# Kernel optimization log

Measured on AMD Instinct MI355X. Metric: run time of the kernel, lower is better.

Reference implementation:

```python
import jax, jax.numpy as jnp
import numpy as np

D_MODEL, D_STATE, DT_RANK = 768, 16, 48
D_INNER = 2 * D_MODEL
B, L = 2, 1024


def ste_clamp(x, lo, hi):
    return x + jax.lax.stop_gradient(jnp.clip(x, lo, hi) - x)


def bitlinear(x, w):
    """BitNet-b1.58-style BitLinear: ternary weights (absmean scale) +
    int8 absmax activation quantization, both with straight-through estimators."""
    eps = 1e-6
    sw = jnp.mean(jnp.abs(w)) + eps
    wn = w / sw
    wq = wn + jax.lax.stop_gradient(jnp.round(jnp.clip(wn, -1.0, 1.0)) - wn)
    sx = 127.0 / (jnp.max(jnp.abs(x), axis=-1, keepdims=True) + eps)
    xn = x * sx
    xq = xn + jax.lax.stop_gradient(jnp.round(jnp.clip(xn, -128.0, 127.0)) - xn)
    return (xq @ wq.T) * (sw / sx)


def bitshift_norm(x, gamma):
    # RMS norm where 1/rms is snapped to a power of two (bit-shift)
    xc = x - jnp.mean(x, axis=-1, keepdims=True)
    var = jnp.mean(xc * xc, axis=-1, keepdims=True)
    rms = jnp.sqrt(var + 1e-6)
    k = jnp.clip(jnp.round(jnp.log2(rms)), 0.0, None)
    inv_rms = 2.0 ** (-k)
    return xc * inv_rms * gamma


def depthwise_conv1d(x, w, b):
    # x: [B, L, C]; w: [C, 1, 4]; b: [C] -> [B, L+3, C] (padding=3 both sides, kernel 4)
    y = jax.lax.conv_general_dilated(
        x.transpose(0, 2, 1), w, window_strides=(1,), padding=[(3, 3)],
        feature_group_count=x.shape[-1], dimension_numbers=("NCH", "OIH", "NCH"))
    return (y + b[None, :, None]).transpose(0, 2, 1)


def dyadic_scan(u, decay):
    # h_t = decay_t * h_{t-1} + u_t along axis=1, vectorized via associative scan
    def combine(c1, c2):
        a1, b1 = c1
        a2, b2 = c2
        return a1 * a2, b1 * a2 + b2
    _, h = jax.lax.associative_scan(combine, (decay, u), axis=1)
    return h


def setup_inputs() -> dict:
    key = jax.random.key(0)
    ks = jax.random.split(key, 8)
    return {
        "hidden_states": jax.random.normal(ks[0], (B, L, D_MODEL), jnp.float32),
        "gamma": jnp.ones((D_MODEL,), jnp.float32),
        "in_proj_w": 0.02 * jax.random.normal(ks[1], (2 * D_INNER, D_MODEL), jnp.float32),
        "conv_w": 0.1 * jax.random.normal(ks[2], (D_INNER, 1, 4), jnp.float32),
        "conv_b": 0.01 * jax.random.normal(ks[3], (D_INNER,), jnp.float32),
        "x_proj_w": 0.02 * jax.random.normal(ks[4], (DT_RANK + 2 * D_STATE, D_INNER), jnp.float32),
        "dt_proj_w": 0.02 * jax.random.normal(ks[5], (D_INNER, DT_RANK), jnp.float32),
        "out_proj_w": 0.02 * jax.random.normal(ks[6], (D_MODEL, D_INNER), jnp.float32),
        "base_decay_nums": jnp.full((D_INNER, D_STATE), 28000.0, jnp.float32),
        "res_gate": jnp.full((1,), 0.01, jnp.float32),
        "decay_shifts": jnp.full((D_INNER, D_STATE), 15.0, jnp.float32),
    }


def reference(hidden_states, gamma, in_proj_w, conv_w, conv_b, x_proj_w,
              dt_proj_w, out_proj_w, base_decay_nums, res_gate, decay_shifts):
    residual = hidden_states
    hs = hidden_states - jnp.mean(hidden_states, axis=-1, keepdims=True)  # module-level centering
    hs = bitshift_norm(hs, gamma)

    xz = bitlinear(hs, in_proj_w)
    x, z = jnp.split(xz, 2, axis=-1)                      # each [B, L, D_INNER]
    x = depthwise_conv1d(x, conv_w, conv_b)[:, :L]
    x = jnp.clip(x, -50.0, 50.0)
    x = 0.5 * (x + jnp.sqrt(x * x + 4.0))                 # smooth softplus-like

    proj = bitlinear(x, x_proj_w)
    dt, B_ssm, C_ssm = jnp.split(proj, [DT_RANK, DT_RANK + D_STATE], axis=-1)
    decay_mod = bitlinear(dt, dt_proj_w)                  # [B, L, D_INNER]

    decay_nums = ste_clamp(base_decay_nums[None, None] + decay_mod[..., None], 0.0, 32000.0)
    dt_val = ste_clamp(0.5 * (decay_mod + jnp.sqrt(decay_mod * decay_mod + 4.0)) * 0.01, 0.0, 0.1)

    u = (x * dt_val)[..., None] * B_ssm[:, :, None, :]    # [B, L, D_INNER, N]
    Bs, Ls, Din, N = u.shape
    u_flat = jnp.clip(u.reshape(Bs, Ls, Din * N), -100.0, 100.0)
    dn_flat = decay_nums.reshape(Bs, Ls, Din * N)
    decay = dn_flat * (2.0 ** (-decay_shifts.reshape(-1)))  # [B, L, Din*N]

    h_flat = jnp.clip(dyadic_scan(u_flat, decay), -1000.0, 1000.0)
    h = h_flat.reshape(Bs, Ls, Din, N)

    y = jnp.einsum("bldn,bln->bld", h, C_ssm)
    y = y * (0.5 * (z / jnp.sqrt(z * z + 1.0) + 1.0))     # smooth sigmoid gate
    out = bitlinear(y, out_proj_w)
    return residual + out * res_gate
```

## Files before the change

kernel.cpp:

```cpp
#include <hip/hip_runtime.h>
#include <hip/hip_bf16.h>
#include <math.h>

#define D_MODEL 768
#define D_STATE 16
#define DT_RANK 48
#define D_INNER 1536
#define XZ_DIM  3072
#define PROJ_DIM 80
#define Bb 2
#define Ll 1024
#define ROWS (Bb*Ll)

#define OFF_PART   0u
#define OFF_SW     256u
#define OFF_WQIN   512u
#define OFF_WQXPT  (OFF_WQIN  + 2359296u)
#define OFF_WQDT   (OFF_WQXPT + 122880u)
#define OFF_WQOUT  (OFF_WQDT  + 73728u)
#define OFF_XQ1    (OFF_WQOUT + 1179648u)
#define OFF_S1     (OFF_XQ1   + 1572864u)
#define OFF_XZ     (OFF_S1    + 2048u)
#define OFF_XS     (OFF_XZ    + 6291456u)
#define OFF_YG     (OFF_XS    + 3145728u)
#define OFF_S2     (OFF_YG    + 3145728u)
#define OFF_PROJ   (OFF_S2    + 2048u)
#define OFF_XQ3    (OFF_PROJ  + 163840u)
#define OFF_S3     (OFF_XQ3   + 98304u)
#define OFF_DMX    (OFF_S3    + 2048u)
#define OFF_XQ4    (OFF_DMX   + 6291456u)
#define OFF_S4     (OFF_XQ4   + 3145728u)

typedef short sh8 __attribute__((ext_vector_type(8)));
typedef float f32x4 __attribute__((ext_vector_type(4)));

#define N_IN_W  (XZ_DIM * D_MODEL)
#define N_XP_W  (PROJ_DIM * D_INNER)
#define N_DT_P  (D_INNER * 64)
#define N_OUT_W (D_MODEL * D_INNER)

__device__ __forceinline__ float blk_sum(float v, float* sm) {
    int tid = threadIdx.x;
    #pragma unroll
    for (int off = 32; off; off >>= 1) v += __shfl_down(v, off);
    __syncthreads();
    if ((tid & 63) == 0) sm[tid >> 6] = v;
    __syncthreads();
    return (sm[0] + sm[1]) + (sm[2] + sm[3]);
}
__device__ __forceinline__ float blk_max(float v, float* sm) {
    int tid = threadIdx.x;
    #pragma unroll
    for (int off = 32; off; off >>= 1) v = fmaxf(v, __shfl_down(v, off));
    __syncthreads();
    if ((tid & 63) == 0) sm[tid >> 6] = v;
    __syncthreads();
    return fmaxf(fmaxf(sm[0], sm[1]), fmaxf(sm[2], sm[3]));
}
__device__ __forceinline__ float clampf(float v, float lo, float hi) {
    return fminf(fmaxf(v, lo), hi);
}
__device__ __forceinline__ void gload_lds16(const __hip_bfloat16* g, __hip_bfloat16* l) {
    __builtin_amdgcn_global_load_lds(
        (const __attribute__((address_space(1))) void*)g,
        (__attribute__((address_space(3))) void*)l, 16, 0, 0);
}
__device__ __forceinline__ float red16_dpp(float v) {
    int t;
    t = __builtin_amdgcn_update_dpp(0, __float_as_int(v), 0xB1,  0xF, 0xF, true);
    v += __int_as_float(t);
    t = __builtin_amdgcn_update_dpp(0, __float_as_int(v), 0x4E,  0xF, 0xF, true);
    v += __int_as_float(t);
    t = __builtin_amdgcn_update_dpp(0, __float_as_int(v), 0x124, 0xF, 0xF, true);
    v += __int_as_float(t);
    t = __builtin_amdgcn_update_dpp(0, __float_as_int(v), 0x128, 0xF, 0xF, true);
    v += __int_as_float(t);
    return v;
}

__global__ __launch_bounds__(256) void absmean_all(
    const float* __restrict__ w0, const float* __restrict__ w1,
    const float* __restrict__ w2, const float* __restrict__ w3,
    float* __restrict__ part) {
    __shared__ float sm[4];
    int bid = blockIdx.x;
    const float* w; int n, sub, nb;
    if (bid < 512)      { w = w0; n = N_IN_W;           sub = bid;       nb = 512; }
    else if (bid < 576) { w = w1; n = N_XP_W;           sub = bid - 512; nb = 64;  }
    else if (bid < 640) { w = w2; n = D_INNER*DT_RANK;  sub = bid - 576; nb = 64;  }
    else                { w = w3; n = N_OUT_W;          sub = bid - 640; nb = 384; }
    float sum = 0.f;
    for (int i = sub * 256 + threadIdx.x; i < n; i += nb * 256)
        sum += fabsf(w[i]);
    sum = blk_sum(sum, sm);
    if (threadIdx.x == 0) part[bid] = sum;
}

__global__ __launch_bounds__(256) void absmean_final4(
    const float* __restrict__ part, float* __restrict__ sw) {
    __shared__ float sm[4];
    int tid = threadIdx.x;
    const int cnt[4] = {512, 64, 64, 384};
    const int off[4] = {0, 512, 576, 640};
    const int ns[4]  = {N_IN_W, N_XP_W, D_INNER*DT_RANK, N_OUT_W};
    #pragma unroll
    for (int m = 0; m < 4; ++m) {
        float v = 0.f;
        for (int i = tid; i < cnt[m]; i += 256) v += part[off[m] + i];
        v = blk_sum(v, sm);
        if (tid == 0) sw[m] = v / (float)ns[m] + 1e-6f;
    }
}

__global__ void quant_all(const float* __restrict__ w_in, const float* __restrict__ w_xp,
                          const float* __restrict__ w_dt, const float* __restrict__ w_out,
                          const float* __restrict__ sw,
                          __hip_bfloat16* __restrict__ wqin, float* __restrict__ wqxpT,
                          __hip_bfloat16* __restrict__ wqdt, __hip_bfloat16* __restrict__ wqout) {
    int idx = blockIdx.x * 256 + threadIdx.x;
    if (idx < N_IN_W) {
        float v = rintf(clampf(w_in[idx] / sw[0], -1.f, 1.f));
        wqin[idx] = __float2bfloat16(v);
    } else if (idx < N_IN_W + N_XP_W) {
        int i = idx - N_IN_W;
        int j = i / D_INNER, k = i % D_INNER;
        wqxpT[k * PROJ_DIM + j] = rintf(clampf(w_xp[i] / sw[1], -1.f, 1.f));
    } else if (idx < N_IN_W + N_XP_W + N_DT_P) {
        int i = idx - N_IN_W - N_XP_W;
        int r = i >> 6, c = i & 63;
        float v = (c < DT_RANK) ? rintf(clampf(w_dt[r * DT_RANK + c] / sw[2], -1.f, 1.f)) : 0.f;
        wqdt[i] = __float2bfloat16(v);
    } else if (idx < N_IN_W + N_XP_W + N_DT_P + N_OUT_W) {
        int i = idx - N_IN_W - N_XP_W - N_DT_P;
        float v = rintf(clampf(w_out[i] / sw[3], -1.f, 1.f));
        wqout[i] = __float2bfloat16(v);
    }
}

__global__ __launch_bounds__(256) void norm_quant(
    const float* __restrict__ x, const float* __restrict__ gamma,
    const float* __restrict__ swp, __hip_bfloat16* __restrict__ xq, float* __restrict__ s1) {
    int row = blockIdx.x, tid = threadIdx.x;
    const float* xr = x + (size_t)row * D_MODEL;
    __shared__ float sm[4];
    float v0 = xr[tid], v1 = xr[tid + 256], v2 = xr[tid + 512];
    float m1 = blk_sum(v0 + v1 + v2, sm) * (1.f / D_MODEL);
    v0 -= m1; v1 -= m1; v2 -= m1;
    float m2 = blk_sum(v0 + v1 + v2, sm) * (1.f / D_MODEL);
    v0 -= m2; v1 -= m2; v2 -= m2;
    float var = blk_sum(v0 * v0 + v1 * v1 + v2 * v2, sm) * (1.f / D_MODEL);
    float rms = sqrtf(var + 1e-6f);
    float k = fmaxf(rintf(log2f(rms)), 0.f);
    float inv = exp2f(-k);
    float g0 = gamma[tid], g1 = gamma[tid + 256], g2 = gamma[tid + 512];
    float h0 = v0 * inv * g0, h1 = v1 * inv * g1, h2 = v2 * inv * g2;
    float mx = blk_max(fmaxf(fabsf(h0), fmaxf(fabsf(h1), fabsf(h2))), sm);
    float sx = 127.f / (mx + 1e-6f);
    __hip_bfloat16* xo = xq + (size_t)row * D_MODEL;
    xo[tid]       = __float2bfloat16(rintf(clampf(h0 * sx, -128.f, 127.f)));
    xo[tid + 256] = __float2bfloat16(rintf(clampf(h1 * sx, -128.f, 127.f)));
    xo[tid + 512] = __float2bfloat16(rintf(clampf(h2 * sx, -128.f, 127.f)));
    if (tid == 0) s1[row] = swp[0] * (mx + 1e-6f) / 127.f;
}

__global__ __launch_bounds__(256) void gate_rowmax_quant_bf16(
    const float* __restrict__ yr, const float* __restrict__ xz,
    const float* __restrict__ swp,
    __hip_bfloat16* __restrict__ xq, float* __restrict__ sout) {
    int row = blockIdx.x, tid = threadIdx.x;
    const float* ir = yr + (size_t)row * D_INNER;
    const float* zr = xz + (size_t)row * XZ_DIM + D_INNER;
    __shared__ float sm[4];
    float v[6];
    #pragma unroll
    for (int k6 = 0; k6 < 6; ++k6) {
        int k = tid + k6 * 256;
        float z = zr[k];
        float g = 0.5f * (z / sqrtf(fmaf(z, z, 1.f)) + 1.f);
        v[k6] = ir[k] * g;
    }
    float mx = 0.f;
    #pragma unroll
    for (int k6 = 0; k6 < 6; ++k6) mx = fmaxf(mx, fabsf(v[k6]));
    mx = blk_max(mx, sm);
    float sx = 127.f / (mx + 1e-6f);
    #pragma unroll
    for (int k6 = 0; k6 < 6; ++k6) {
        int k = tid + k6 * 256;
        xq[(size_t)row * D_INNER + k] = __float2bfloat16(rintf(clampf(v[k6] * sx, -128.f, 127.f)));
    }
    if (tid == 0) sout[row] = swp[0] * (mx + 1e-6f) / 127.f;
}

template<int MF, int NF>
__global__ __launch_bounds__(256) void gemm_mfma(
    const __hip_bfloat16* __restrict__ A, const __hip_bfloat16* __restrict__ W,
    const float* __restrict__ s, float* __restrict__ C,
    int M, int N, int K,
    const float* __restrict__ resid, const float* __restrict__ rg) {
    constexpr int BM = MF * 32, BN = NF * 32;
    __shared__ __hip_bfloat16 smA[BM * 32];
    __shared__ __hip_bfloat16 smB[BN * 32];
    const int tid = threadIdx.x;
    const int w = tid >> 6, lane = tid & 63;
    const int bm = blockIdx.y * BM, bn = blockIdx.x * BN;
    const int wr = (w >> 1) * (MF * 16), wc = (w & 1) * (NF * 16);
    const int fr = lane & 15, fq = lane >> 4;
    const int srow = lane >> 2;
    const int scol = (lane & 3) * 8;

    f32x4 acc[MF][NF];
    #pragma unroll
    for (int i = 0; i < MF; ++i)
        #pragma unroll
        for (int j = 0; j < NF; ++j)
            acc[i][j] = (f32x4){0.f, 0.f, 0.f, 0.f};

    for (int k0 = 0; k0 < K; k0 += 32) {
        #pragma unroll
        for (int q = 0; q < BM / 64; ++q) {
            int rr = (w * (BM / 64) + q) * 16;
            gload_lds16(A + (size_t)(bm + rr + srow) * K + k0 + scol, &smA[rr * 32]);
        }
        if (w < (BN / 16)) {
            int rr = w * 16;
            gload_lds16(W + (size_t)(bn + rr + srow) * K + k0 + scol, &smB[rr * 32]);
        }
        __syncthreads();
        sh8 af[MF], bfr[NF];
        #pragma unroll
        for (int i = 0; i < MF; ++i)
            af[i] = *(const sh8*)&smA[(wr + i * 16 + fr) * 32 + fq * 8];
        #pragma unroll
        for (int j = 0; j < NF; ++j)
            bfr[j] = *(const sh8*)&smB[(wc + j * 16 + fr) * 32 + fq * 8];
        #pragma unroll
        for (int i = 0; i < MF; ++i)
            #pragma unroll
            for (int j = 0; j < NF; ++j)
                acc[i][j] = __builtin_amdgcn_mfma_f32_16x16x32_bf16(af[i], bfr[j], acc[i][j], 0, 0, 0);
        __syncthreads();
    }
    const float rgv = resid ? rg[0] : 0.f;
    #pragma unroll
    for (int i = 0; i < MF; ++i) {
        #pragma unroll
        for (int q = 0; q < 4; ++q) {
            int r = bm + wr + i * 16 + fq * 4 + q;
            float sc = s[r];
            #pragma unroll
            for (int j = 0; j < NF; ++j) {
                int col = bn + wc + j * 16 + fr;
                float v = acc[i][j][q] * sc;
                size_t o = (size_t)r * N + col;
                if (resid) v = resid[o] + v * rgv;
                C[o] = v;
            }
        }
    }
}

#define CR2 2
__global__ __launch_bounds__(512) void conv_xproj(
    const float* __restrict__ xz, const float* __restrict__ cw, const float* __restrict__ cb,
    const float* __restrict__ swp,
    const float* __restrict__ wT,
    float* __restrict__ xs,
    float* __restrict__ proj, __hip_bfloat16* __restrict__ xq3, float* __restrict__ s3) {
    int row0 = blockIdx.x * CR2;
    int tid = threadIdx.x;
    int w = tid >> 6, lane = tid & 63;
    int r = w >> 2, q = w & 3;
    __shared__ float sm8[8];
    __shared__ float a[CR2][D_INNER];
    __shared__ float psum[8][CR2 * PROJ_DIM];
    __shared__ float pvL[CR2][PROJ_DIM];
    __shared__ float s2s[CR2];

    int row = row0 + r;
    int b = row >> 10, l = row & 1023;
    float v[6];
    float mx = 0.f;
    #pragma unroll
    for (int k = 0; k < 6; ++k) {
        int c = q * 384 + lane + k * 64;
        float acc = cb[c];
        #pragma unroll
        for (int t = 0; t < 4; ++t) {
            int tt = l - 3 + t;
            if (tt >= 0)
                acc = fmaf(cw[c * 4 + t], xz[(size_t)(b * Ll + tt) * XZ_DIM + c], acc);
        }
        acc = clampf(acc, -50.f, 50.f);
        v[k] = 0.5f * (acc + sqrtf(fmaf(acc, acc, 4.f)));
        mx = fmaxf(mx, fabsf(v[k]));
    }
    #pragma unroll
    for (int off = 32; off; off >>= 1) mx = fmaxf(mx, __shfl_xor(mx, off));
    if (lane == 0) sm8[w] = mx;
    __syncthreads();
    mx = fmaxf(fmaxf(sm8[r * 4 + 0], sm8[r * 4 + 1]), fmaxf(sm8[r * 4 + 2], sm8[r * 4 + 3]));
    float sx = 127.f / (mx + 1e-6f);
    #pragma unroll
    for (int k = 0; k < 6; ++k) {
        int c = q * 384 + lane + k * 64;
        xs[(size_t)row * D_INNER + c] = v[k];
        a[r][c] = rintf(clampf(v[k] * sx, -128.f, 127.f));
    }
    if (lane == 0 && q == 0) s2s[r] = swp[1] * (mx + 1e-6f) / 127.f;
    __syncthreads();

    for (int task = tid; task < CR2 * PROJ_DIM * 8; task += 512) {
        int h = task / (CR2 * PROJ_DIM);
        int o = task - h * (CR2 * PROJ_DIM);
        int rr = o / PROJ_DIM, col = o - rr * PROJ_DIM;
        int k0 = h * 192;
        float a0 = 0.f, a1 = 0.f;
        for (int k = k0; k < k0 + 96; ++k)
            a0 = fmaf(a[rr][k], wT[k * PROJ_DIM + col], a0);
        for (int k = k0 + 96; k < k0 + 192; ++k)
            a1 = fmaf(a[rr][k], wT[k * PROJ_DIM + col], a1);
        psum[h][o] = a0 + a1;
    }
    __syncthreads();
    for (int o = tid; o < CR2 * PROJ_DIM; o += 512) {
        int rr = o / PROJ_DIM, col = o - rr * PROJ_DIM;
        float pv = (((psum[0][o] + psum[1][o]) + (psum[2][o] + psum[3][o])) +
                    ((psum[4][o] + psum[5][o]) + (psum[6][o] + psum[7][o]))) * s2s[rr];
        proj[(size_t)(row0 + rr) * PROJ_DIM + col] = pv;
        pvL[rr][col] = pv;
    }
    __syncthreads();
    if (w < CR2) {
        float pvv = (lane < DT_RANK) ? pvL[w][lane] : 0.f;
        float av = fabsf(pvv);
        #pragma unroll
        for (int off = 32; off; off >>= 1) av = fmaxf(av, __shfl_xor(av, off));
        float sxd = 127.f / (av + 1e-6f);
        float qv = (lane < DT_RANK) ? rintf(clampf(pvv * sxd, -128.f, 127.f)) : 0.f;
        xq3[(size_t)(row0 + w) * 64 + lane] = __float2bfloat16(qv);
        if (lane == 0) s3[row0 + w] = swp[2] * (av + 1e-6f) / 127.f;
    }
}

__global__ __launch_bounds__(256) void gemm_dt_mfma(
    const __hip_bfloat16* __restrict__ A, const __hip_bfloat16* __restrict__ W,
    const float* __restrict__ s, const float* __restrict__ xs,
    float2* __restrict__ dmx) {
    __shared__ __hip_bfloat16 smA[64 * 32];
    __shared__ __hip_bfloat16 smB[64 * 32];
    __shared__ float t0[64][65];
    __shared__ float t1[64][65];
    const int tid = threadIdx.x;
    const int w = tid >> 6, lane = tid & 63;
    const int bm = blockIdx.y * 64, bn = blockIdx.x * 64;
    const int wr = (w >> 1) * 32, wc = (w & 1) * 32;
    const int fr = lane & 15, fq = lane >> 4;
    const int srow = lane >> 2;
    const int scol = (lane & 3) * 8;

    f32x4 acc[2][2];
    #pragma unroll
    for (int i = 0; i < 2; ++i)
        #pragma unroll
        for (int j = 0; j < 2; ++j)
            acc[i][j] = (f32x4){0.f, 0.f, 0.f, 0.f};

    #pragma unroll
    for (int k0 = 0; k0 < 64; k0 += 32) {
        {
            int rr = w * 16;
            gload_lds16(A + (size_t)(bm + rr + srow) * 64 + k0 + scol, &smA[rr * 32]);
            gload_lds16(W + (size_t)(bn + rr + srow) * 64 + k0 + scol, &smB[rr * 32]);
        }
        __syncthreads();
        sh8 af[2], bfr[2];
        #pragma unroll
        for (int i = 0; i < 2; ++i)
            af[i] = *(const sh8*)&smA[(wr + i * 16 + fr) * 32 + fq * 8];
        #pragma unroll
        for (int j = 0; j < 2; ++j)
            bfr[j] = *(const sh8*)&smB[(wc + j * 16 + fr) * 32 + fq * 8];
        #pragma unroll
        for (int i = 0; i < 2; ++i)
            #pragma unroll
            for (int j = 0; j < 2; ++j)
                acc[i][j] = __builtin_amdgcn_mfma_f32_16x16x32_bf16(af[i], bfr[j], acc[i][j], 0, 0, 0);
        __syncthreads();
    }
    #pragma unroll
    for (int i = 0; i < 2; ++i) {
        #pragma unroll
        for (int q = 0; q < 4; ++q) {
            int r = wr + i * 16 + fq * 4 + q;
            float sc = s[bm + r];
            #pragma unroll
            for (int j = 0; j < 2; ++j) {
                int col = wc + j * 16 + fr;
                t0[col][r] = acc[i][j][q] * sc;
            }
        }
    }
    #pragma unroll
    for (int it = 0; it < 16; ++it) {
        int idx = tid + it * 256;
        int rr = idx >> 6, cc = idx & 63;
        t1[cc][rr] = xs[(size_t)(bm + rr) * D_INNER + bn + cc];
    }
    __syncthreads();
    int b = bm >> 10, lbase = bm & 1023;
    #pragma unroll
    for (int it = 0; it < 16; ++it) {
        int idx = tid + it * 256;
        int dd = idx >> 6, ll = idx & 63;
        float dm = t0[dd][ll];
        float xv = t1[dd][ll];
        float dtv = clampf(0.5f * (dm + sqrtf(fmaf(dm, dm, 4.f))) * 0.01f, 0.f, 0.1f);
        size_t dst = ((size_t)(bn + dd) * Bb + b) * Ll + lbase + ll;
        dmx[dst] = make_float2(dm, xv * dtv);
    }
}

#define NCHUNK 32
#define CLEN   32
#define PADIDX(i) ((i) + ((i) >> 5))
__global__ __launch_bounds__(512) void scan_chunked(
    const float2* __restrict__ dmx,
    const float* __restrict__ proj,
    const float* __restrict__ base, const float* __restrict__ shifts,
    float* __restrict__ yg) {
    int bid = blockIdx.x;
    int d = bid >> 1, b = bid & 1;
    int tid = threadIdx.x;
    int chunk = tid >> 4, n = tid & 15;
    __shared__ float2 dmxL[Ll + Ll / 32];
    __shared__ float Ps[NCHUNK][16];
    __shared__ float Hs[NCHUNK][16];
    __shared__ float Cin[NCHUNK][16];
    size_t tbase = (size_t)bid * Ll;
    for (int i = tid; i < Ll; i += 512)
        dmxL[PADIDX(i)] = dmx[tbase + i];
    float bs_n  = base[d * D_STATE + n];
    float asc_n = exp2f(-shifts[d * D_STATE + n]);
    __syncthreads();
    float P = 1.f, h = 0.f;
    int l0 = chunk * CLEN;
    int pbase = PADIDX(l0);
    const float* projR = proj + (size_t)(b * Ll) * PROJ_DIM;
    #pragma unroll
    for (int s4 = 0; s4 < CLEN; s4 += 4) {
        float Bv[4];
        #pragma unroll
        for (int j = 0; j < 4; ++j)
            Bv[j] = projR[(size_t)(l0 + s4 + j) * PROJ_DIM + DT_RANK + n];
        #pragma unroll
        for (int j = 0; j < 4; ++j) {
            float2 dx = dmxL[pbase + s4 + j];
            float u = clampf(dx.y * Bv[j], -100.f, 100.f);
            float a = clampf(bs_n + dx.x, 0.f, 32000.f) * asc_n;
            h = fmaf(a, h, u);
            P *= a;
        }
    }
    Ps[chunk][n] = P;
    Hs[chunk][n] = h;
    __syncthreads();
    if (tid < 16) {
        float carry = 0.f;
        for (int c = 0; c < NCHUNK; ++c) {
            Cin[c][tid] = carry;
            carry = fmaf(Ps[c][tid], carry, Hs[c][tid]);
        }
    }
    __syncthreads();
    h = Cin[chunk][n];
    float* ygr = yg + (size_t)(b * Ll) * D_INNER + d;
    #pragma unroll
    for (int s4 = 0; s4 < CLEN; s4 += 4) {
        float Bv[4], Cv[4];
        #pragma unroll
        for (int j = 0; j < 4; ++j) {
            size_t pr = (size_t)(l0 + s4 + j) * PROJ_DIM;
            Bv[j] = projR[pr + DT_RANK + n];
            Cv[j] = projR[pr + DT_RANK + D_STATE + n];
        }
        #pragma unroll
        for (int j = 0; j < 4; ++j) {
            float2 dx = dmxL[pbase + s4 + j];
            float u = clampf(dx.y * Bv[j], -100.f, 100.f);
            float a = clampf(bs_n + dx.x, 0.f, 32000.f) * asc_n;
            h = fmaf(a, h, u);
            float hc = clampf(h, -1000.f, 1000.f);
            float y = red16_dpp(hc * Cv[j]);
            if (n == 0) {
                ygr[(size_t)(l0 + s4 + j) * D_INNER] = y;
            }
        }
    }
}

extern "C" void kernel_launch(void* const* d_in, const int* in_sizes, int n_in,
                              void* d_out, int out_size, void* d_ws, size_t ws_size,
                              hipStream_t stream) {
    const float* hs    = (const float*)d_in[0];
    const float* gamma = (const float*)d_in[1];
    const float* w_in  = (const float*)d_in[2];
    const float* cw    = (const float*)d_in[3];
    const float* cb    = (const float*)d_in[4];
    const float* w_xp  = (const float*)d_in[5];
    const float* w_dt  = (const float*)d_in[6];
    const float* w_out = (const float*)d_in[7];
    const float* base  = (const float*)d_in[8];
    const float* rg    = (const float*)d_in[9];
    const float* shifts= (const float*)d_in[10];
    float* ws  = (float*)d_ws;
    float* out = (float*)d_out;

    __hip_bfloat16* wqin  = (__hip_bfloat16*)(ws + OFF_WQIN);
    __hip_bfloat16* wqdt  = (__hip_bfloat16*)(ws + OFF_WQDT);
    __hip_bfloat16* wqout = (__hip_bfloat16*)(ws + OFF_WQOUT);
    __hip_bfloat16* xq1   = (__hip_bfloat16*)(ws + OFF_XQ1);
    __hip_bfloat16* xq3   = (__hip_bfloat16*)(ws + OFF_XQ3);
    __hip_bfloat16* xq4   = (__hip_bfloat16*)(ws + OFF_XQ4);
    float2*         dmx   = (float2*)(ws + OFF_DMX);

    absmean_all<<<1024, 256, 0, stream>>>(w_in, w_xp, w_dt, w_out, ws + OFF_S2);
    absmean_final4<<<1, 256, 0, stream>>>(ws + OFF_S2, ws + OFF_SW);
    const int n_tot = N_IN_W + N_XP_W + N_DT_P + N_OUT_W;
    quant_all<<<(n_tot + 255) / 256, 256, 0, stream>>>(
        w_in, w_xp, w_dt, w_out, ws + OFF_SW,
        wqin, ws + OFF_WQXPT, wqdt, wqout);
    norm_quant<<<ROWS, 256, 0, stream>>>(hs, gamma, ws + OFF_SW + 0, xq1, ws + OFF_S1);
    gemm_mfma<4, 2><<<dim3(XZ_DIM / 64, ROWS / 128), 256, 0, stream>>>(
        xq1, wqin, ws + OFF_S1, ws + OFF_XZ,
        ROWS, XZ_DIM, D_MODEL, nullptr, nullptr);
    conv_xproj<<<ROWS / CR2, 512, 0, stream>>>(ws + OFF_XZ, cw, cb, ws + OFF_SW,
                                               ws + OFF_WQXPT, ws + OFF_XS,
                                               ws + OFF_PROJ, xq3, ws + OFF_S3);
    gemm_dt_mfma<<<dim3(D_INNER / 64, ROWS / 64), 256, 0, stream>>>(
        xq3, wqdt, ws + OFF_S3, ws + OFF_XS, dmx);
    scan_chunked<<<Bb * D_INNER, 512, 0, stream>>>(
        dmx, ws + OFF_PROJ, base, shifts, ws + OFF_YG);
    gate_rowmax_quant_bf16<<<ROWS, 256, 0, stream>>>(ws + OFF_YG, ws + OFF_XZ,
                                                     ws + OFF_SW + 3, xq4, ws + OFF_S4);
    gemm_mfma<2, 2><<<dim3(D_MODEL / 64, ROWS / 64), 256, 0, stream>>>(
        xq4, wqout, ws + OFF_S4, out,
        ROWS, D_MODEL, D_INNER, hs, rg);
}
```

Baseline: 193.0 us.

## Give each scan thread four states with vector loads and retile out-proj GEMM

The chunked scan now has each thread own four of the sixteen state channels. It uses 64 chunks of 16 steps and 256-thread blocks instead of 16 threads per chunk at 512 threads. B and C values are read as float4 vectors, and the per-step C reduction becomes four in-register FMAs plus a two-step DPP reduction instead of a four-step one. The aim is to cut the per-step shuffle cost and redundant scalar global loads, at the cost of more registers and a longer serial carry pass across 64 chunks. Separately, the output-projection GEMM switches to a narrower tile template with twice as many column blocks to raise occupancy.

Measured after the change: 189.9 us. About the same (-1.6%).

```diff
diff --git a/kernel.cpp b/kernel.cpp
--- a/kernel.cpp
+++ b/kernel.cpp
@@ -64,18 +64,6 @@
     __builtin_amdgcn_global_load_lds(
         (const __attribute__((address_space(1))) void*)g,
         (__attribute__((address_space(3))) void*)l, 16, 0, 0);
-}
-__device__ __forceinline__ float red16_dpp(float v) {
-    int t;
-    t = __builtin_amdgcn_update_dpp(0, __float_as_int(v), 0xB1,  0xF, 0xF, true);
-    v += __int_as_float(t);
-    t = __builtin_amdgcn_update_dpp(0, __float_as_int(v), 0x4E,  0xF, 0xF, true);
-    v += __int_as_float(t);
-    t = __builtin_amdgcn_update_dpp(0, __float_as_int(v), 0x124, 0xF, 0xF, true);
-    v += __int_as_float(t);
-    t = __builtin_amdgcn_update_dpp(0, __float_as_int(v), 0x128, 0xF, 0xF, true);
-    v += __int_as_float(t);
-    return v;
 }
 
 __global__ __launch_bounds__(256) void absmean_all(
@@ -421,10 +409,10 @@
     }
 }
 
-#define NCHUNK 32
-#define CLEN   32
+#define NCHUNK 64
+#define CLEN   16
 #define PADIDX(i) ((i) + ((i) >> 5))
-__global__ __launch_bounds__(512) void scan_chunked(
+__global__ __launch_bounds__(256) void scan_chunked(
     const float2* __restrict__ dmx,
     const float* __restrict__ proj,
     const float* __restrict__ base, const float* __restrict__ shifts,
@@ -432,38 +420,43 @@
     int bid = blockIdx.x;
     int d = bid >> 1, b = bid & 1;
     int tid = threadIdx.x;
-    int chunk = tid >> 4, n = tid & 15;
+    int chunk = tid >> 2, sub = tid & 3;
     __shared__ float2 dmxL[Ll + Ll / 32];
     __shared__ float Ps[NCHUNK][16];
     __shared__ float Hs[NCHUNK][16];
     __shared__ float Cin[NCHUNK][16];
     size_t tbase = (size_t)bid * Ll;
-    for (int i = tid; i < Ll; i += 512)
+    for (int i = tid; i < Ll; i += 256)
         dmxL[PADIDX(i)] = dmx[tbase + i];
-    float bs_n  = base[d * D_STATE + n];
-    float asc_n = exp2f(-shifts[d * D_STATE + n]);
-    __syncthreads();
-    float P = 1.f, h = 0.f;
+    float bs[4], asc[4], h[4], P[4];
+    #pragma unroll
+    for (int j = 0; j < 4; ++j) {
+        int n = sub * 4 + j;
+        bs[j]  = base[d * D_STATE + n];
+        asc[j] = exp2f(-shifts[d * D_STATE + n]);
+        h[j] = 0.f;
+        P[j] = 1.f;
+    }
+    __syncthreads();
     int l0 = chunk * CLEN;
     int pbase = PADIDX(l0);
     const float* projR = proj + (size_t)(b * Ll) * PROJ_DIM;
-    #pragma unroll
-    for (int s4 = 0; s4 < CLEN; s4 += 4) {
-        float Bv[4];
-        #pragma unroll
-        for (int j = 0; j < 4; ++j)
-            Bv[j] = projR[(size_t)(l0 + s4 + j) * PROJ_DIM + DT_RANK + n];
+    for (int s = 0; s < CLEN; ++s) {
+        float2 dx = dmxL[pbase + s];
+        f32x4 Bv = *(const f32x4*)&projR[(size_t)(l0 + s) * PROJ_DIM + DT_RANK + sub * 4];
         #pragma unroll
         for (int j = 0; j < 4; ++j) {
-            float2 dx = dmxL[pbase + s4 + j];
             float u = clampf(dx.y * Bv[j], -100.f, 100.f);
-            float a = clampf(bs_n + dx.x, 0.f, 32000.f) * asc_n;
-            h = fmaf(a, h, u);
-            P *= a;
-        }
-    }
-    Ps[chunk][n] = P;
-    Hs[chunk][n] = h;
+            float a = clampf(bs[j] + dx.x, 0.f, 32000.f) * asc[j];
+            h[j] = fmaf(a, h[j], u);
+            P[j] *= a;
+        }
+    }
+    #pragma unroll
+    for (int j = 0; j < 4; ++j) {
+        Ps[chunk][sub * 4 + j] = P[j];
+        Hs[chunk][sub * 4 + j] = h[j];
+    }
     __syncthreads();
     if (tid < 16) {
         float carry = 0.f;
@@ -473,28 +466,30 @@
         }
     }
     __syncthreads();
-    h = Cin[chunk][n];
+    #pragma unroll
+    for (int j = 0; j < 4; ++j) h[j] = Cin[chunk][sub * 4 + j];
     float* ygr = yg + (size_t)(b * Ll) * D_INNER + d;
-    #pragma unroll
-    for (int s4 = 0; s4 < CLEN; s4 += 4) {
-        float Bv[4], Cv[4];
+    for (int s = 0; s < CLEN; ++s) {
+        float2 dx = dmxL[pbase + s];
+        size_t pr = (size_t)(l0 + s) * PROJ_DIM + DT_RANK + sub * 4;
+        f32x4 Bv = *(const f32x4*)&projR[pr];
+        f32x4 Cv = *(const f32x4*)&projR[pr + D_STATE];
+        float y = 0.f;
         #pragma unroll
         for (int j = 0; j < 4; ++j) {
-            size_t pr = (size_t)(l0 + s4 + j) * PROJ_DIM;
-            Bv[j] = projR[pr + DT_RANK + n];
-            Cv[j] = projR[pr + DT_RANK + D_STATE + n];
-        }
-        #pragma unroll
-        for (int j = 0; j < 4; ++j) {
-            float2 dx = dmxL[pbase + s4 + j];
             float u = clampf(dx.y * Bv[j], -100.f, 100.f);
-            float a = clampf(bs_n + dx.x, 0.f, 32000.f) * asc_n;
-            h = fmaf(a, h, u);
-            float hc = clampf(h, -1000.f, 1000.f);
-            float y = red16_dpp(hc * Cv[j]);
-            if (n == 0) {
-                ygr[(size_t)(l0 + s4 + j) * D_INNER] = y;
-            }
+            float a = clampf(bs[j] + dx.x, 0.f, 32000.f) * asc[j];
+            h[j] = fmaf(a, h[j], u);
+            float hc = clampf(h[j], -1000.f, 1000.f);
+            y = fmaf(hc, Cv[j], y);
+        }
+        int t;
+        t = __builtin_amdgcn_update_dpp(0, __float_as_int(y), 0xB1, 0xF, 0xF, true);
+        y += __int_as_float(t);
+        t = __builtin_amdgcn_update_dpp(0, __float_as_int(y), 0x4E, 0xF, 0xF, true);
+        y += __int_as_float(t);
+        if (sub == 0) {
+            ygr[(size_t)(l0 + s) * D_INNER] = y;
         }
     }
 }
@@ -539,11 +534,11 @@
                                                ws + OFF_PROJ, xq3, ws + OFF_S3);
     gemm_dt_mfma<<<dim3(D_INNER / 64, ROWS / 64), 256, 0, stream>>>(
         xq3, wqdt, ws + OFF_S3, ws + OFF_XS, dmx);
-    scan_chunked<<<Bb * D_INNER, 512, 0, stream>>>(
+    scan_chunked<<<Bb * D_INNER, 256, 0, stream>>>(
         dmx, ws + OFF_PROJ, base, shifts, ws + OFF_YG);
     gate_rowmax_quant_bf16<<<ROWS, 256, 0, stream>>>(ws + OFF_YG, ws + OFF_XZ,
                                                      ws + OFF_SW + 3, xq4, ws + OFF_S4);
-    gemm_mfma<2, 2><<<dim3(D_MODEL / 64, ROWS / 64), 256, 0, stream>>>(
+    gemm_mfma<2, 1><<<dim3(D_MODEL / 32, ROWS / 64), 256, 0, stream>>>(
         xq4, wqout, ws + OFF_S4, out,
         ROWS, D_MODEL, D_INNER, hs, rg);
 }
```
